# Kernel tuning notes

Hardware: AMD Instinct MI355X
Metric: run time of the kernel (lower is better)

## Reference

```python
import jax, jax.numpy as jnp
import numpy as np
from jax import lax

# Module config (matches init_kwargs): mode='swta', patchwise=True, w_nrm=True, k=1, alpha=1
COUT, CIN, KH, KW = 32, 16, 3, 3
STRIDE = 1
K_TEMP = 1.0


def setup_inputs() -> dict:
    key = jax.random.key(0)
    k1, k2 = jax.random.split(key)
    x = jax.random.normal(k1, (16, CIN, 256, 256), dtype=jnp.float32)
    # xavier_normal_: std = sqrt(2/(fan_in+fan_out)), fan_in=CIN*KH*KW, fan_out=COUT*KH*KW
    std = float(np.sqrt(2.0 / (CIN * KH * KW + COUT * KH * KW)))
    weight = jax.random.normal(k2, (COUT, CIN, KH, KW), dtype=jnp.float32) * std
    bias = jnp.zeros((COUT,), dtype=jnp.float32)
    return {"x": x, "weight": weight, "bias": bias}


def _unfold(x, kh, kw, sh, sw):
    # torch F.unfold: output [B, C*kh*kw, L], patch features ordered (c, kh, kw)
    B, C, H, W = x.shape
    Ho = (H - kh) // sh + 1
    Wo = (W - kw) // sw + 1
    cols = [x[:, :, i:i + (Ho - 1) * sh + 1:sh, j:j + (Wo - 1) * sw + 1:sw]
            for i in range(kh) for j in range(kw)]  # each [B,C,Ho,Wo]
    p = jnp.stack(cols, axis=2)  # [B, C, kh*kw, Ho, Wo]
    return p.reshape(B, C * kh * kw, Ho * Wo)


def reference(x, weight, bias):
    # --- compute_activation: weight-normalized conv2d (act = Identity) ---
    nrm = jnp.sqrt((weight ** 2).sum(axis=(1, 2, 3), keepdims=True))
    nrm = jnp.where(nrm == 0, jnp.ones_like(nrm), nrm)
    w = weight / nrm
    y = lax.conv_general_dilated(
        x, w, window_strides=(STRIDE, STRIDE), padding='VALID',
        dimension_numbers=('NCHW', 'OIHW', 'NCHW')) + bias[None, :, None, None]

    # --- SWTA Hebbian update (torch: under no_grad, stored into delta_w buffer) ---
    x_unf = _unfold(x, KH, KW, STRIDE, STRIDE)               # [B, CKK, L]
    x_flat = x_unf.transpose(0, 2, 1).reshape(-1, x_unf.shape[1])  # [B*L, CKK]
    r = jax.nn.softmax(y * K_TEMP, axis=1).transpose(1, 0, 2, 3)   # [O, B, Ho, Wo]
    r_sum = jnp.abs(r).sum(axis=(1, 2, 3), keepdims=True)
    r_sum = jnp.where(r_sum == 0, jnp.ones_like(r_sum), r_sum)
    cr = (jnp.abs(r) / r_sum) * r                             # [O, B, Ho, Wo]
    cr_flat = cr.reshape(COUT, -1)                            # [O, B*L]
    dec = cr_flat.sum(axis=1, keepdims=True) * weight.reshape(COUT, -1)
    delta_w = (cr_flat @ x_flat - dec).reshape(weight.shape)  # [O, CIN, KH, KW]

    return y, delta_w
```

## Files before the change

kernel.cpp:

```cpp
#include <hip/hip_runtime.h>


typedef unsigned short ushort_t;
typedef __attribute__((ext_vector_type(8)))  short  short8v;
typedef __attribute__((ext_vector_type(4)))  float  float4v;
typedef __attribute__((ext_vector_type(16))) float  float16v;

struct __attribute__((packed, aligned(4))) f4a { float x,y,z,w; };
struct __attribute__((packed, aligned(4))) f2a { float x,y; };
struct __attribute__((packed, aligned(2))) u2a { ushort_t x,y; };

#define BATCH 16
#define CIN   16
#define H     256
#define W     256
#define HW    (H*W)
#define OCH   32
#define HO    254
#define WO    254
#define LPOS  (HO*WO)
#define YELEMS (BATCH*OCH*LPOS)
#define KFEAT 144
#define NROWS (BATCH*HO)
#define NCHUNK (NROWS*8)
#define GRIDA 1016
#define NSLAB GRIDA
#define NGRP  8
#define SLABS_PER_GRP 127

#define TCOLS 36

#define WS_RSUM 0
#define WS_R2   32
#define WS_ACC  64
#define WS_MODE 4672
#define WS_WNB  4680
#define WS_PART 8192
#define WS_PART2 (8192 + NSLAB*4608)
#define WS_NEED ((size_t)(WS_PART2 + NGRP*4608)*4)

__device__ __forceinline__ float bf2f(ushort_t u){
  union{unsigned u; float f;} c; c.u = ((unsigned)u) << 16; return c.f;
}
__device__ __forceinline__ ushort_t f2bf(float f){
  union{float f; unsigned u;} c; c.f = f;
  unsigned x = c.u;
  return (ushort_t)((x + 0x7fffu + ((x >> 16) & 1u)) >> 16);
}
__device__ __forceinline__ unsigned as_u(float f){
  union{float f; unsigned u;} c; c.f = f; return c.u;
}
__device__ __forceinline__ void gload_lds16(const float* g, void* l){
  __builtin_amdgcn_global_load_lds(
      (const __attribute__((address_space(1))) void*)g,
      (__attribute__((address_space(3))) void*)l, 16, 0, 0);
}

__global__ __launch_bounds__(256) void hebb_prep(const ushort_t* __restrict__ x,
                                                 const ushort_t* __restrict__ w,
                                                 int* __restrict__ mode,
                                                 float* __restrict__ ws){
  int tid = threadIdx.x;
  int bad = 0;
  for (int i = tid; i < 16384; i += 256){
    unsigned e = ((unsigned)x[i] >> 7) & 0xFFu;
    bad |= (e >= 0x8Cu) ? 1 : 0;
  }
  unsigned long long m = __ballot(bad);
  __shared__ unsigned long long sm[4];
  __shared__ int mode_s;
  int wv = tid >> 6;
  if ((tid & 63) == 0) sm[wv] = m;
  __syncthreads();
  if (tid == 0){
    int md = ((sm[0] | sm[1] | sm[2] | sm[3]) != 0ULL) ? 1 : 0;
    *mode = md; mode_s = md;
  }
  __syncthreads();
  const int fp32 = mode_s;
  const float* wf = (const float*)w;
  __shared__ float inv_s[OCH];
  if (tid < OCH){
    float s = 0.f;
    for (int k = 0; k < KFEAT; k++){
      float v = fp32 ? wf[tid*KFEAT + k] : bf2f(w[tid*KFEAT + k]);
      s += v*v;
    }
    float nrm = sqrtf(s);
    inv_s[tid] = (nrm == 0.f) ? 1.f : (1.f/nrm);
  }
  __syncthreads();
  ushort_t* wnb = (ushort_t*)(ws + WS_WNB);
  for (int i = tid; i < 4608; i += 256){
    int o = i & 31, rest = i >> 5;
    int ij = rest >> 4, c = rest & 15;
    int k = c*9 + ij;
    float v = fp32 ? wf[o*KFEAT + k] : bf2f(w[o*KFEAT + k]);
    wnb[i] = f2bf(v * inv_s[o]);
    ws[WS_ACC + i] = 0.f;
  }
  if (tid < 64) ws[WS_RSUM + tid] = 0.f;
}

template<int FP32>
__global__ __launch_bounds__(256, 2) void hebb_passAB(
    const void* __restrict__ xv_, const void* __restrict__ bias_,
    const int* __restrict__ mode, const float* __restrict__ ws,
    float* __restrict__ rsum_g, float* __restrict__ r2sum_g,
    void* __restrict__ yout_, float* __restrict__ partial, int do_hebb){
  if (*mode != FP32) return;
  __shared__ __align__(16) float xtile[4][1792];
  __shared__ __align__(16) ushort_t r2t[4][32*40];
  __shared__ float red_s[64];
  float* redp = &xtile[0][0];
  int tid = threadIdx.x;
  if (tid < 64) red_s[tid] = 0.f;
  __syncthreads();
  int wave = tid >> 6, lane = tid & 63;
  int pos = lane & 31, half = lane >> 5;
  int quad = lane >> 4, l16 = lane & 15;

  const ushort_t* wnb = (const ushort_t*)(ws + WS_WNB);
  short8v wa[9];
  #pragma unroll
  for (int ij = 0; ij < 9; ij++){
    union{ushort_t s[8]; short8v v;} pk;
    #pragma unroll
    for (int i = 0; i < 8; i++)
      pk.s[i] = wnb[(ij*16 + half*8 + i)*32 + pos];
    wa[ij] = pk.v;
  }
  float bv[16];
  #pragma unroll
  for (int r = 0; r < 16; r++){
    int och = (r&3) + 8*(r>>2) + 4*half;
    bv[r] = FP32 ? ((const float*)bias_)[och] : bf2f(((const ushort_t*)bias_)[och]);
  }
  float rsA[16];
  #pragma unroll
  for (int r = 0; r < 16; r++) rsA[r] = 0.f;
  float r2B0 = 0.f, r2B1 = 0.f;

  int goff[7], qcol[7];
  #pragma unroll
  for (int i = 0; i < 7; i++){
    int slot = i*64 + lane; slot = (slot > 431) ? 431 : slot;
    int rr = slot/9, q = slot - 9*rr;
    int c = rr/3, ii = rr - 3*c;
    goff[i] = c*HW + ii*W;
    qcol[i] = q*4;
  }

  float4v hacc[18];
  #pragma unroll
  for (int i = 0; i < 18; i++) hacc[i] = (float4v){0.f,0.f,0.f,0.f};

  ushort_t* t2 = r2t[wave];
  float* tw = &xtile[wave][0];

  for (int cc0 = blockIdx.x*4 + wave; cc0 < NCHUNK; cc0 += GRIDA*4){
    int cc = __builtin_amdgcn_readfirstlane(cc0);
    int row = cc >> 3, sub = cc & 7;
    int b = row / HO, ho = row - b*HO;
    int wo0 = sub << 5;
    int wo = wo0 + pos;
    int tail = (sub == 7);

    float16v av;
    #pragma unroll
    for (int r = 0; r < 16; r++) av[r] = bv[r];

    if (FP32){
      const float* xb = (const float*)xv_ + (size_t)b*(CIN*HW) + (size_t)ho*W;
      #pragma unroll
      for (int i = 0; i < 7; i++){
        int col = wo0 + qcol[i]; col = (col > 252) ? 252 : col;
        gload_lds16(xb + goff[i] + col, (char*)tw + i*1024);
      }
      asm volatile("s_waitcnt vmcnt(0)" ::: "memory");

      #pragma unroll
      for (int ij = 0; ij < 9; ij++){
        const int ii = ij/3, jj = ij - 3*ii;
        unsigned g[8];
        #pragma unroll
        for (int i2 = 0; i2 < 8; i2++)
          g[i2] = as_u(tw[((half*8 + i2)*3 + ii)*TCOLS + pos + jj]) + 0x8000u;
        union{unsigned u[4]; short8v v;} pk;
        pk.u[0] = __builtin_amdgcn_perm(g[1], g[0], 0x07060302u);
        pk.u[1] = __builtin_amdgcn_perm(g[3], g[2], 0x07060302u);
        pk.u[2] = __builtin_amdgcn_perm(g[5], g[4], 0x07060302u);
        pk.u[3] = __builtin_amdgcn_perm(g[7], g[6], 0x07060302u);
        av = __builtin_amdgcn_mfma_f32_32x32x16_bf16(wa[ij], pk.v, av, 0, 0, 0);
      }
    } else {
      #pragma unroll
      for (int ij = 0; ij < 9; ij++){
        const int ii = ij/3, jj = ij - 3*ii;
        int wcol = wo + jj; wcol = (wcol < 256) ? wcol : 255;
        size_t a0 = (size_t)b*(CIN*HW) + (size_t)(half*8)*HW + (size_t)(ho+ii)*W + wcol;
        const ushort_t* xp = (const ushort_t*)xv_;
        union{ushort_t s[8]; short8v v;} pk;
        #pragma unroll
        for (int i2 = 0; i2 < 8; i2++)
          pk.s[i2] = xp[a0 + (size_t)i2*HW];
        av = __builtin_amdgcn_mfma_f32_32x32x16_bf16(wa[ij], pk.v, av, 0, 0, 0);
      }
    }

    int valid = (wo < WO) ? 1 : 0;
    if (valid){
      size_t yb = (size_t)b*(OCH*(size_t)LPOS) + (size_t)(half*4)*LPOS
                + (size_t)ho*WO + wo;
      #pragma unroll
      for (int r = 0; r < 16; r++){
        size_t yi = yb + (size_t)(((r&3) + 8*(r>>2)))*LPOS;
        if (FP32) ((float*)yout_)[yi] = av[r];
        else      ((ushort_t*)yout_)[yi] = f2bf(av[r]);
      }
    }

    float m = -3.0e38f;
    #pragma unroll
    for (int r = 0; r < 16; r++) m = fmaxf(m, av[r]);
    m = fmaxf(m, __shfl_xor(m, 32));
    float s = 0.f;
    #pragma unroll
    for (int r = 0; r < 16; r++){ float e = __expf(av[r] - m); av[r] = e; s += e; }
    s += __shfl_xor(s, 32);
    float inv = valid ? (1.f/s) : 0.f;

    #pragma unroll
    for (int r = 0; r < 16; r++){
      float rr = av[r]*inv;
      rsA[r] += rr;
      int och = (r&3) + 8*(r>>2) + 4*half;
      t2[och*40 + pos] = f2bf(rr*rr);
    }

    short8v a0 = *(const short8v*)(t2 + l16*40      + quad*8);
    short8v a1 = *(const short8v*)(t2 + (16+l16)*40 + quad*8);
    {
      float p0 = 0.f, p1 = 0.f;
      #pragma unroll
      for (int i = 0; i < 8; i++){
        p0 += bf2f((ushort_t)a0[i]);
        p1 += bf2f((ushort_t)a1[i]);
      }
      r2B0 += p0; r2B1 += p1;
    }

    if (do_hebb){
      if (FP32){
        #pragma unroll
        for (int n = 0; n < 9; n++){
          int kh = n*16 + l16, c = kh/9, ij2 = kh - 9*c, ii = ij2/3, jj = ij2 - 3*ii;
          const float* hp = tw + (c*3 + ii)*TCOLS + jj + quad*8;
          unsigned f[8];
          #pragma unroll
          for (int i = 0; i < 8; i++) f[i] = as_u(hp[i]);
          union{unsigned u[4]; short8v v;} pk;
          pk.u[0] = __builtin_amdgcn_perm(f[1], f[0], 0x07060302u);
          pk.u[1] = __builtin_amdgcn_perm(f[3], f[2], 0x07060302u);
          pk.u[2] = __builtin_amdgcn_perm(f[5], f[4], 0x07060302u);
          pk.u[3] = __builtin_amdgcn_perm(f[7], f[6], 0x07060302u);
          hacc[n]   = __builtin_amdgcn_mfma_f32_16x16x32_bf16(a0, pk.v, hacc[n],   0,0,0);
          hacc[9+n] = __builtin_amdgcn_mfma_f32_16x16x32_bf16(a1, pk.v, hacc[9+n], 0,0,0);
        }
      } else {
        int xbase = b*(CIN*HW) + ho*W + wo0;
        #pragma unroll
        for (int n = 0; n < 9; n++){
          int kh = n*16 + l16, c = kh/9, ij2 = kh - 9*c, ii = ij2/3, jj = ij2 - 3*ii;
          int ko = (c*H + ii)*W + jj;
          const ushort_t* xp = (const ushort_t*)xv_ + (size_t)(xbase + ko + quad*8);
          union{ushort_t s[8]; short8v v;} pk;
          if (tail && quad == 3){
            u2a u0 = *(const u2a*)xp, u1 = *(const u2a*)(xp+2), u2 = *(const u2a*)(xp+4);
            pk.s[0]=u0.x; pk.s[1]=u0.y; pk.s[2]=u1.x; pk.s[3]=u1.y;
            pk.s[4]=u2.x; pk.s[5]=u2.y; pk.s[6]=0; pk.s[7]=0;
          } else {
            u2a u0 = *(const u2a*)xp,   u1 = *(const u2a*)(xp+2);
            u2a u2 = *(const u2a*)(xp+4), u3 = *(const u2a*)(xp+6);
            pk.s[0]=u0.x; pk.s[1]=u0.y; pk.s[2]=u1.x; pk.s[3]=u1.y;
            pk.s[4]=u2.x; pk.s[5]=u2.y; pk.s[6]=u3.x; pk.s[7]=u3.y;
          }
          hacc[n]   = __builtin_amdgcn_mfma_f32_16x16x32_bf16(a0, pk.v, hacc[n],   0,0,0);
          hacc[9+n] = __builtin_amdgcn_mfma_f32_16x16x32_bf16(a1, pk.v, hacc[9+n], 0,0,0);
        }
      }
    }
  }

  #pragma unroll
  for (int r = 0; r < 16; r++){
    float a = rsA[r];
    #pragma unroll
    for (int off = 1; off < 32; off <<= 1)
      a += __shfl_xor(a, off);
    if (pos == 0){
      int och = (r&3) + 8*(r>>2) + 4*half;
      atomicAdd(&red_s[och], a);
    }
  }
  r2B0 += __shfl_xor(r2B0, 16); r2B0 += __shfl_xor(r2B0, 32);
  r2B1 += __shfl_xor(r2B1, 16); r2B1 += __shfl_xor(r2B1, 32);
  if (lane < 16){
    atomicAdd(&red_s[32 + lane],      r2B0);
    atomicAdd(&red_s[32 + 16 + lane], r2B1);
  }
  __syncthreads();
  if (tid < 32)      atomicAdd(rsum_g  + tid,      red_s[tid]);
  else if (tid < 64) atomicAdd(r2sum_g + (tid-32), red_s[tid]);

  if (do_hebb){
    for (int wv = 0; wv < 4; wv++){
      if (wave == wv){
        #pragma unroll
        for (int mi = 0; mi < 2; mi++)
          #pragma unroll
          for (int n = 0; n < 9; n++)
            #pragma unroll
            for (int rg = 0; rg < 4; rg++){
              int o  = mi*16 + quad*4 + rg;
              int kh = n*16 + l16;
              if (wv == 0) redp[o*KFEAT + kh]  = hacc[mi*9+n][rg];
              else         redp[o*KFEAT + kh] += hacc[mi*9+n][rg];
            }
      }
      __syncthreads();
    }
    float* myp = partial + (size_t)blockIdx.x*4608;
    for (int i = tid; i < 4608; i += 256) myp[i] = redp[i];
  }
}

__global__ __launch_bounds__(256) void hebb_red(const float* __restrict__ partial,
                                                float* __restrict__ partial2){
  int t = blockIdx.x*256 + threadIdx.x;
  if (t >= NGRP*4608) return;
  int g = t / 4608, col = t - g*4608;
  const float* p = partial + (size_t)g*SLABS_PER_GRP*4608 + col;
  float s0=0.f, s1=0.f, s2=0.f, s3=0.f;
  int j = 0;
  for (; j + 4 <= SLABS_PER_GRP; j += 4){
    s0 += p[(size_t)(j  )*4608];
    s1 += p[(size_t)(j+1)*4608];
    s2 += p[(size_t)(j+2)*4608];
    s3 += p[(size_t)(j+3)*4608];
  }
  for (; j < SLABS_PER_GRP; j++) s0 += p[(size_t)j*4608];
  partial2[t] = ((s0+s1)+(s2+s3));
}

template<int FP32>
__global__ __launch_bounds__(256) void hebb_passB_fb(
    const void* __restrict__ xv_, const int* __restrict__ mode,
    const float* __restrict__ ws, const void* __restrict__ ybf_,
    float* __restrict__ acc_g){
  if (*mode != FP32) return;
  __shared__ __align__(16) ushort_t crs[32*128];
  __shared__ __align__(16) ushort_t xs[144*128];
  __shared__ float rsinv_s[32];
  int tid = threadIdx.x;
  if (tid < 32){
    float rs = ws[WS_RSUM + tid];
    rsinv_s[tid] = (rs == 0.f) ? 1.f : (1.f/rs);
  }
  __syncthreads();

  float4v av[18];
  #pragma unroll
  for (int i = 0; i < 18; i++) av[i] = (float4v){0.f,0.f,0.f,0.f};
  int wave = tid >> 6, lane = tid & 63;
  int quad = lane >> 4, l16 = lane & 15;
  int t = tid & 127, kh0 = tid >> 7;

  for (int s = blockIdx.x; s < NROWS*2; s += (int)gridDim.x){
    int row = s >> 1, half = s & 1;
    int b = row / HO, ho = row - b*HO;
    int wo0 = half << 7;
    int tlen = half ? (WO - 128) : 128;
    size_t xoff = (size_t)b*(CIN*HW) + (size_t)ho*W + wo0;
    bool tvalid = t < tlen;

    #pragma unroll
    for (int it = 0; it < 72; it++){
      const int kh = 2*it + kh0;
      const int c = kh/9, ij = kh - 9*c, ii = ij/3, jj = ij - 3*ii;
      size_t gi = xoff + (size_t)(c*H + ii)*W + jj + t;
      ushort_t val;
      if (FP32) val = tvalid ? f2bf(((const float*)xv_)[gi]) : (ushort_t)0;
      else      val = tvalid ? ((const ushort_t*)xv_)[gi]    : (ushort_t)0;
      xs[kh*128 + t] = val;
    }
    if (tid < 128){
      if (tvalid){
        float r[32];
        size_t yb = (size_t)b*(OCH*(size_t)LPOS) + (size_t)ho*WO + wo0 + tid;
        float m = -3.0e38f;
        #pragma unroll
        for (int o = 0; o < 32; o++){
          float v = FP32 ? ((const float*)ybf_)[yb + (size_t)o*LPOS]
                         : bf2f(((const ushort_t*)ybf_)[yb + (size_t)o*LPOS]);
          r[o] = v; m = fmaxf(m, v);
        }
        float ssum = 0.f;
        #pragma unroll
        for (int o = 0; o < 32; o++){ r[o] = __expf(r[o]-m); ssum += r[o]; }
        float inv = 1.f/ssum;
        #pragma unroll
        for (int o = 0; o < 32; o++) r[o] *= inv;
        #pragma unroll
        for (int o = 0; o < 32; o++) crs[o*128 + tid] = f2bf(r[o]*r[o]*rsinv_s[o]);
      } else {
        #pragma unroll
        for (int o = 0; o < 32; o++) crs[o*128 + tid] = 0;
      }
    }
    __syncthreads();

    int t0 = wave*32;
    short8v a0 = *(const short8v*)(crs + l16*128      + t0 + quad*8);
    short8v a1 = *(const short8v*)(crs + (16+l16)*128 + t0 + quad*8);
    #pragma unroll
    for (int n = 0; n < 9; n++){
      short8v bfr = *(const short8v*)(xs + (n*16 + l16)*128 + t0 + quad*8);
      av[n]   = __builtin_amdgcn_mfma_f32_16x16x32_bf16(a0, bfr, av[n],   0,0,0);
      av[9+n] = __builtin_amdgcn_mfma_f32_16x16x32_bf16(a1, bfr, av[9+n], 0,0,0);
    }
    __syncthreads();
  }

  #pragma unroll
  for (int mi = 0; mi < 2; mi++)
    #pragma unroll
    for (int n = 0; n < 9; n++)
      #pragma unroll
      for (int rg = 0; rg < 4; rg++){
        int o  = mi*16 + quad*4 + rg;
        int kh = n*16 + l16;
        atomicAdd(acc_g + o*KFEAT + kh, av[mi*9+n][rg]);
      }
}

__global__ __launch_bounds__(256) void hebb_fin(const ushort_t* __restrict__ w,
    const int* __restrict__ mode, const float* __restrict__ ws,
    const float* __restrict__ partial2, int use_rbuf, void* __restrict__ dout){
  int tid = blockIdx.x*256 + threadIdx.x;
  if (tid >= 4608) return;
  const int fp32 = *mode;
  int o = tid / KFEAT;
  float rs = ws[WS_RSUM + o];
  rs = (rs == 0.f) ? 1.f : rs;
  float base;
  if (use_rbuf){
    float s = 0.f;
    #pragma unroll
    for (int j = 0; j < NGRP; j++)
      s += partial2[(size_t)j*4608 + tid];
    base = s / rs;
  } else {
    base = ws[WS_ACC + tid];
  }
  float crsum = ws[WS_R2 + o] / rs;
  float wv = fp32 ? ((const float*)w)[tid] : bf2f(w[tid]);
  float d = base - crsum * wv;
  if (fp32) ((float*)dout)[(size_t)YELEMS + tid] = d;
  else      ((ushort_t*)dout)[(size_t)YELEMS + tid] = f2bf(d);
}

extern "C" void kernel_launch(void* const* d_in, const int* in_sizes, int n_in,
                              void* d_out, int out_size, void* d_ws, size_t ws_size,
                              hipStream_t stream){
  const void* x    = d_in[0];
  const ushort_t* w = (const ushort_t*)d_in[1];
  const void* bias = d_in[2];
  float* ws   = (float*)d_ws;
  int*   mode = (int*)(ws + WS_MODE);
  float* part = ws + WS_PART;
  float* part2 = ws + WS_PART2;
  int use_rbuf = (ws_size >= WS_NEED) ? 1 : 0;

  hebb_prep<<<1, 256, 0, stream>>>((const ushort_t*)x, w, mode, ws);
  hebb_passAB<0><<<GRIDA, 256, 0, stream>>>(x, bias, mode, ws,
                                            ws + WS_RSUM, ws + WS_R2, d_out,
                                            part, use_rbuf);
  hebb_passAB<1><<<GRIDA, 256, 0, stream>>>(x, bias, mode, ws,
                                            ws + WS_RSUM, ws + WS_R2, d_out,
                                            part, use_rbuf);
  if (use_rbuf){
    hebb_red<<<144, 256, 0, stream>>>(part, part2);
  } else {
    hebb_passB_fb<0><<<512, 256, 0, stream>>>(x, mode, ws, d_out, ws + WS_ACC);
    hebb_passB_fb<1><<<512, 256, 0, stream>>>(x, mode, ws, d_out, ws + WS_ACC);
  }
  hebb_fin<<<18, 256, 0, stream>>>(w, mode, ws, part2, use_rbuf, d_out);
}
```

Measured before the change: 287.2 us.

## Double-buffer x tile prefetch in fused pass and merge fp32/bf16 kernel launches

The fp32 path now keeps two LDS x-tile buffers per wave and issues async global-to-LDS loads for the next chunk before computing the current one, waiting only on the older loads. The loop has a fixed trip count of 8, since NCHUNK equals GRIDA*4*8. The two templated launches that checked a mode flag are merged into one kernel that branches at runtime, which removes one launch of early-exiting blocks. LDS use for xtile doubles, which may reduce occupancy, and the runtime branch means both paths are compiled into one kernel, which may raise register pressure.

```diff
diff --git a/kernel.cpp b/kernel.cpp
--- a/kernel.cpp
+++ b/kernel.cpp
@@ -7,7 +7,6 @@
 typedef __attribute__((ext_vector_type(16))) float  float16v;
 
 struct __attribute__((packed, aligned(4))) f4a { float x,y,z,w; };
-struct __attribute__((packed, aligned(4))) f2a { float x,y; };
 struct __attribute__((packed, aligned(2))) u2a { ushort_t x,y; };
 
 #define BATCH 16
@@ -102,17 +101,16 @@
   if (tid < 64) ws[WS_RSUM + tid] = 0.f;
 }
 
-template<int FP32>
 __global__ __launch_bounds__(256, 2) void hebb_passAB(
     const void* __restrict__ xv_, const void* __restrict__ bias_,
     const int* __restrict__ mode, const float* __restrict__ ws,
     float* __restrict__ rsum_g, float* __restrict__ r2sum_g,
     void* __restrict__ yout_, float* __restrict__ partial, int do_hebb){
-  if (*mode != FP32) return;
-  __shared__ __align__(16) float xtile[4][1792];
+  const int fp32 = *mode;
+  __shared__ __align__(16) float xtile[4][2][1792];
   __shared__ __align__(16) ushort_t r2t[4][32*40];
   __shared__ float red_s[64];
-  float* redp = &xtile[0][0];
+  float* redp = &xtile[0][0][0];
   int tid = threadIdx.x;
   if (tid < 64) red_s[tid] = 0.f;
   __syncthreads();
@@ -134,7 +132,7 @@
   #pragma unroll
   for (int r = 0; r < 16; r++){
     int och = (r&3) + 8*(r>>2) + 4*half;
-    bv[r] = FP32 ? ((const float*)bias_)[och] : bf2f(((const ushort_t*)bias_)[och]);
+    bv[r] = fp32 ? ((const float*)bias_)[och] : bf2f(((const ushort_t*)bias_)[och]);
   }
   float rsA[16];
   #pragma unroll
@@ -156,28 +154,46 @@
   for (int i = 0; i < 18; i++) hacc[i] = (float4v){0.f,0.f,0.f,0.f};
 
   ushort_t* t2 = r2t[wave];
-  float* tw = &xtile[wave][0];
-
-  for (int cc0 = blockIdx.x*4 + wave; cc0 < NCHUNK; cc0 += GRIDA*4){
-    int cc = __builtin_amdgcn_readfirstlane(cc0);
-    int row = cc >> 3, sub = cc & 7;
-    int b = row / HO, ho = row - b*HO;
-    int wo0 = sub << 5;
-    int wo = wo0 + pos;
-    int tail = (sub == 7);
-
-    float16v av;
-    #pragma unroll
-    for (int r = 0; r < 16; r++) av[r] = bv[r];
-
-    if (FP32){
+  const int cc0 = blockIdx.x*4 + wave;
+
+  if (fp32){
+    {
+      int cc = __builtin_amdgcn_readfirstlane(cc0);
+      int row = cc >> 3, sub = cc & 7;
+      int b = row / HO, ho = row - b*HO, wo0 = sub << 5;
       const float* xb = (const float*)xv_ + (size_t)b*(CIN*HW) + (size_t)ho*W;
+      char* twn = (char*)&xtile[wave][0][0];
       #pragma unroll
       for (int i = 0; i < 7; i++){
         int col = wo0 + qcol[i]; col = (col > 252) ? 252 : col;
-        gload_lds16(xb + goff[i] + col, (char*)tw + i*1024);
-      }
-      asm volatile("s_waitcnt vmcnt(0)" ::: "memory");
+        gload_lds16(xb + goff[i] + col, twn + i*1024);
+      }
+    }
+    for (int kk = 0; kk < 8; kk++){
+      int cc = __builtin_amdgcn_readfirstlane(cc0 + kk*(GRIDA*4));
+      int row = cc >> 3, sub = cc & 7;
+      int b = row / HO, ho = row - b*HO;
+      int wo0 = sub << 5;
+      int wo = wo0 + pos;
+      float* tw = &xtile[wave][kk & 1][0];
+
+      if (kk < 7){
+        int cn = __builtin_amdgcn_readfirstlane(cc0 + (kk+1)*(GRIDA*4));
+        int rown = cn >> 3, subn = cn & 7;
+        int bn = rown / HO, hon = rown - bn*HO, won0 = subn << 5;
+        const float* xbn = (const float*)xv_ + (size_t)bn*(CIN*HW) + (size_t)hon*W;
+        char* twn = (char*)&xtile[wave][(kk+1) & 1][0];
+        #pragma unroll
+        for (int i = 0; i < 7; i++){
+          int col = won0 + qcol[i]; col = (col > 252) ? 252 : col;
+          gload_lds16(xbn + goff[i] + col, twn + i*1024);
+        }
+      }
+      asm volatile("s_waitcnt vmcnt(7)" ::: "memory");
+
+      float16v av;
+      #pragma unroll
+      for (int r = 0; r < 16; r++) av[r] = bv[r];
 
       #pragma unroll
       for (int ij = 0; ij < 9; ij++){
@@ -193,65 +209,49 @@
         pk.u[3] = __builtin_amdgcn_perm(g[7], g[6], 0x07060302u);
         av = __builtin_amdgcn_mfma_f32_32x32x16_bf16(wa[ij], pk.v, av, 0, 0, 0);
       }
-    } else {
-      #pragma unroll
-      for (int ij = 0; ij < 9; ij++){
-        const int ii = ij/3, jj = ij - 3*ii;
-        int wcol = wo + jj; wcol = (wcol < 256) ? wcol : 255;
-        size_t a0 = (size_t)b*(CIN*HW) + (size_t)(half*8)*HW + (size_t)(ho+ii)*W + wcol;
-        const ushort_t* xp = (const ushort_t*)xv_;
-        union{ushort_t s[8]; short8v v;} pk;
-        #pragma unroll
-        for (int i2 = 0; i2 < 8; i2++)
-          pk.s[i2] = xp[a0 + (size_t)i2*HW];
-        av = __builtin_amdgcn_mfma_f32_32x32x16_bf16(wa[ij], pk.v, av, 0, 0, 0);
-      }
-    }
-
-    int valid = (wo < WO) ? 1 : 0;
-    if (valid){
-      size_t yb = (size_t)b*(OCH*(size_t)LPOS) + (size_t)(half*4)*LPOS
-                + (size_t)ho*WO + wo;
+
+      int valid = (wo < WO) ? 1 : 0;
+      if (valid){
+        size_t yb = (size_t)b*(OCH*(size_t)LPOS) + (size_t)(half*4)*LPOS
+                  + (size_t)ho*WO + wo;
+        #pragma unroll
+        for (int r = 0; r < 16; r++){
+          size_t yi = yb + (size_t)(((r&3) + 8*(r>>2)))*LPOS;
+          ((float*)yout_)[yi] = av[r];
+        }
+      }
+
+      float m = -3.0e38f;
+      #pragma unroll
+      for (int r = 0; r < 16; r++) m = fmaxf(m, av[r]);
+      m = fmaxf(m, __shfl_xor(m, 32));
+      float s = 0.f;
+      #pragma unroll
+      for (int r = 0; r < 16; r++){ float e = __expf(av[r] - m); av[r] = e; s += e; }
+      s += __shfl_xor(s, 32);
+      float inv = valid ? (1.f/s) : 0.f;
+
       #pragma unroll
       for (int r = 0; r < 16; r++){
-        size_t yi = yb + (size_t)(((r&3) + 8*(r>>2)))*LPOS;
-        if (FP32) ((float*)yout_)[yi] = av[r];
-        else      ((ushort_t*)yout_)[yi] = f2bf(av[r]);
-      }
-    }
-
-    float m = -3.0e38f;
-    #pragma unroll
-    for (int r = 0; r < 16; r++) m = fmaxf(m, av[r]);
-    m = fmaxf(m, __shfl_xor(m, 32));
-    float s = 0.f;
-    #pragma unroll
-    for (int r = 0; r < 16; r++){ float e = __expf(av[r] - m); av[r] = e; s += e; }
-    s += __shfl_xor(s, 32);
-    float inv = valid ? (1.f/s) : 0.f;
-
-    #pragma unroll
-    for (int r = 0; r < 16; r++){
-      float rr = av[r]*inv;
-      rsA[r] += rr;
-      int och = (r&3) + 8*(r>>2) + 4*half;
-      t2[och*40 + pos] = f2bf(rr*rr);
-    }
-
-    short8v a0 = *(const short8v*)(t2 + l16*40      + quad*8);
-    short8v a1 = *(const short8v*)(t2 + (16+l16)*40 + quad*8);
-    {
-      float p0 = 0.f, p1 = 0.f;
-      #pragma unroll
-      for (int i = 0; i < 8; i++){
-        p0 += bf2f((ushort_t)a0[i]);
-        p1 += bf2f((ushort_t)a1[i]);
-      }
-      r2B0 += p0; r2B1 += p1;
-    }
-
-    if (do_hebb){
-      if (FP32){
+        float rr = av[r]*inv;
+        rsA[r] += rr;
+        int och = (r&3) + 8*(r>>2) + 4*half;
+        t2[och*40 + pos] = f2bf(rr*rr);
+      }
+
+      short8v a0 = *(const short8v*)(t2 + l16*40      + quad*8);
+      short8v a1 = *(const short8v*)(t2 + (16+l16)*40 + quad*8);
+      {
+        float p0 = 0.f, p1 = 0.f;
+        #pragma unroll
+        for (int i = 0; i < 8; i++){
+          p0 += bf2f((ushort_t)a0[i]);
+          p1 += bf2f((ushort_t)a1[i]);
+        }
+        r2B0 += p0; r2B1 += p1;
+      }
+
+      if (do_hebb){
         #pragma unroll
         for (int n = 0; n < 9; n++){
           int kh = n*16 + l16, c = kh/9, ij2 = kh - 9*c, ii = ij2/3, jj = ij2 - 3*ii;
@@ -267,7 +267,76 @@
           hacc[n]   = __builtin_amdgcn_mfma_f32_16x16x32_bf16(a0, pk.v, hacc[n],   0,0,0);
           hacc[9+n] = __builtin_amdgcn_mfma_f32_16x16x32_bf16(a1, pk.v, hacc[9+n], 0,0,0);
         }
-      } else {
+      }
+    }
+  } else {
+    for (int kk = 0; kk < 8; kk++){
+      int cc = __builtin_amdgcn_readfirstlane(cc0 + kk*(GRIDA*4));
+      int row = cc >> 3, sub = cc & 7;
+      int b = row / HO, ho = row - b*HO;
+      int wo0 = sub << 5;
+      int wo = wo0 + pos;
+      int tail = (sub == 7);
+
+      float16v av;
+      #pragma unroll
+      for (int r = 0; r < 16; r++) av[r] = bv[r];
+
+      #pragma unroll
+      for (int ij = 0; ij < 9; ij++){
+        const int ii = ij/3, jj = ij - 3*ii;
+        int wcol = wo + jj; wcol = (wcol < 256) ? wcol : 255;
+        size_t a0i = (size_t)b*(CIN*HW) + (size_t)(half*8)*HW + (size_t)(ho+ii)*W + wcol;
+        const ushort_t* xp = (const ushort_t*)xv_;
+        union{ushort_t s[8]; short8v v;} pk;
+        #pragma unroll
+        for (int i2 = 0; i2 < 8; i2++)
+          pk.s[i2] = xp[a0i + (size_t)i2*HW];
+        av = __builtin_amdgcn_mfma_f32_32x32x16_bf16(wa[ij], pk.v, av, 0, 0, 0);
+      }
+
+      int valid = (wo < WO) ? 1 : 0;
+      if (valid){
+        size_t yb = (size_t)b*(OCH*(size_t)LPOS) + (size_t)(half*4)*LPOS
+                  + (size_t)ho*WO + wo;
+        #pragma unroll
+        for (int r = 0; r < 16; r++){
+          size_t yi = yb + (size_t)(((r&3) + 8*(r>>2)))*LPOS;
+          ((ushort_t*)yout_)[yi] = f2bf(av[r]);
+        }
+      }
+
+      float m = -3.0e38f;
+      #pragma unroll
+      for (int r = 0; r < 16; r++) m = fmaxf(m, av[r]);
+      m = fmaxf(m, __shfl_xor(m, 32));
+      float s = 0.f;
+      #pragma unroll
+      for (int r = 0; r < 16; r++){ float e = __expf(av[r] - m); av[r] = e; s += e; }
+      s += __shfl_xor(s, 32);
+      float inv = valid ? (1.f/s) : 0.f;
+
+      #pragma unroll
+      for (int r = 0; r < 16; r++){
+        float rr = av[r]*inv;
+        rsA[r] += rr;
+        int och = (r&3) + 8*(r>>2) + 4*half;
+        t2[och*40 + pos] = f2bf(rr*rr);
+      }
+
+      short8v a0 = *(const short8v*)(t2 + l16*40      + quad*8);
+      short8v a1 = *(const short8v*)(t2 + (16+l16)*40 + quad*8);
+      {
+        float p0 = 0.f, p1 = 0.f;
+        #pragma unroll
+        for (int i = 0; i < 8; i++){
+          p0 += bf2f((ushort_t)a0[i]);
+          p1 += bf2f((ushort_t)a1[i]);
+        }
+        r2B0 += p0; r2B1 += p1;
+      }
+
+      if (do_hebb){
         int xbase = b*(CIN*HW) + ho*W + wo0;
         #pragma unroll
         for (int n = 0; n < 9; n++){
@@ -483,12 +552,9 @@
   int use_rbuf = (ws_size >= WS_NEED) ? 1 : 0;
 
   hebb_prep<<<1, 256, 0, stream>>>((const ushort_t*)x, w, mode, ws);
-  hebb_passAB<0><<<GRIDA, 256, 0, stream>>>(x, bias, mode, ws,
-                                            ws + WS_RSUM, ws + WS_R2, d_out,
-                                            part, use_rbuf);
-  hebb_passAB<1><<<GRIDA, 256, 0, stream>>>(x, bias, mode, ws,
-                                            ws + WS_RSUM, ws + WS_R2, d_out,
-                                            part, use_rbuf);
+  hebb_passAB<<<GRIDA, 256, 0, stream>>>(x, bias, mode, ws,
+                                         ws + WS_RSUM, ws + WS_R2, d_out,
+                                         part, use_rbuf);
   if (use_rbuf){
     hebb_red<<<144, 256, 0, stream>>>(part, part2);
   } else {
```

Result: slower. 300.8 us (+4.8%).
